# Optimization experiments

Hardware: AMD Instinct MI355X
Metric: run time of the kernel (lower is better)

The kernel has to match this reference:

```python
import jax, jax.numpy as jnp
import numpy as np

B, N, NPOINT, NSAMPLE = 8, 16384, 512, 64
RADIUS = 0.1
C_IN = 64
DIMS = [64, 64, 128]


def setup_inputs() -> dict:
    key = jax.random.key(0)
    ks = jax.random.split(key, 8)
    xyz = jax.random.uniform(ks[0], (B, N, 3), jnp.float32)          # points in unit cube
    features = jax.random.normal(ks[1], (B, C_IN, N), jnp.float32)   # (B, C, N) per GroupGatherByIndex
    dims = [3 + C_IN] + DIMS                                         # use_xyz_feature adds 3
    out = {"xyz": xyz, "features": features}
    for i in range(3):
        out[f"W{i+1}"] = jax.random.normal(ks[2 + i], (dims[i], dims[i + 1]), jnp.float32) / np.sqrt(dims[i])
        out[f"b{i+1}"] = jnp.zeros((dims[i + 1],), jnp.float32)
    return out


def furthest_point_sampling(xyz, npoint):
    # Iterative FPS starting at index 0 (matches CUDA kernel semantics).
    Bq, Nq, _ = xyz.shape
    barange = jnp.arange(Bq)

    def step(carry, _):
        dists, last = carry
        p = xyz[barange, last]                       # (B, 3)
        d = jnp.sum((xyz - p[:, None, :]) ** 2, -1)  # (B, N)
        dists = jnp.minimum(dists, d)
        nxt = jnp.argmax(dists, axis=1).astype(jnp.int32)
        return (dists, nxt), nxt

    init = (jnp.full((Bq, Nq), 1e10, xyz.dtype), jnp.zeros((Bq,), jnp.int32))
    _, idxs = jax.lax.scan(step, init, None, length=npoint - 1)
    return jnp.concatenate([jnp.zeros((Bq, 1), jnp.int32), idxs.T], axis=1)  # (B, npoint)


def ball_query(new_xyz, xyz, radius, nsample):
    # For each centroid, first nsample in-ball indices (ascending), padded with first hit.
    Nq = xyz.shape[1]
    d2 = jnp.sum((new_xyz[:, :, None, :] - xyz[:, None, :, :]) ** 2, -1)  # (B, npoint, N)
    cand = jnp.where(d2 < radius * radius, jnp.arange(Nq, dtype=jnp.int32), Nq)
    cand = jnp.sort(cand, axis=-1)[..., :nsample]                          # (B, npoint, nsample)
    first = jnp.where(cand[..., :1] == Nq, 0, cand[..., :1])
    return jnp.where(cand == Nq, first, cand)


def reference(xyz, features, W1, b1, W2, b2, W3, b3):
    fps_idx = furthest_point_sampling(xyz, NPOINT)                  # (B, npoint)
    new_xyz = jax.vmap(lambda p, i: p[i])(xyz, fps_idx)             # (B, npoint, 3)
    idx = ball_query(new_xyz, xyz, RADIUS, NSAMPLE)                 # (B, npoint, nsample)
    grouped_xyz = jax.vmap(lambda p, i: p[i])(xyz, idx)             # (B, npoint, nsample, 3)
    centered = grouped_xyz - new_xyz[:, :, None, :]                 # centroid subtract
    feats_n = jnp.transpose(features, (0, 2, 1))                    # (B, N, C)
    grouped_f = jax.vmap(lambda f, i: f[i])(feats_n, idx)           # (B, npoint, nsample, C)
    h = jnp.concatenate([centered, grouped_f], axis=-1)             # (B, npoint, nsample, 3+C)
    for W, b in ((W1, b1), (W2, b2), (W3, b3)):                     # pointwise 1x1-conv MLP + ReLU
        h = jax.nn.relu(h @ W + b)
    return jnp.max(h, axis=2)                                       # max-pool over nsample -> (B, npoint, C_out)
```

## Files before the change

kernel.cpp:

```cpp
#include <hip/hip_runtime.h>

#define NB 8
#define NPTS 16384
#define NPOINT 512
#define NSAMPLE 64
#define CIN 64

typedef float v2f __attribute__((ext_vector_type(2)));

template <int CTRL>
__device__ __forceinline__ float dpp_f(float x) {
    int xi = __builtin_bit_cast(int, x);
    int yi = __builtin_amdgcn_update_dpp(xi, xi, CTRL, 0xF, 0xF, false);
    return __builtin_bit_cast(float, yi);
}
template <int CTRL>
__device__ __forceinline__ int dpp_i(int x) {
    return __builtin_amdgcn_update_dpp(x, x, CTRL, 0xF, 0xF, false);
}

__device__ __forceinline__ float wave_max_f(float x) {
    x = fmaxf(x, dpp_f<0x111>(x));
    x = fmaxf(x, dpp_f<0x112>(x));
    x = fmaxf(x, dpp_f<0x114>(x));
    x = fmaxf(x, dpp_f<0x118>(x));
    x = fmaxf(x, dpp_f<0x142>(x));
    x = fmaxf(x, dpp_f<0x143>(x));
    return x;
}
__device__ __forceinline__ int wave_min_i(int x) {
    x = min(x, dpp_i<0x111>(x));
    x = min(x, dpp_i<0x112>(x));
    x = min(x, dpp_i<0x114>(x));
    x = min(x, dpp_i<0x118>(x));
    x = min(x, dpp_i<0x142>(x));
    x = min(x, dpp_i<0x143>(x));
    return x;
}

#define CMB(va, ia, vb, ib) { bool t_ = ((vb) > (va)) || (((vb) == (va)) && ((ib) < (ia))); \
                              if (t_) { (va) = (vb); (ia) = (ib); } }

__global__ __launch_bounds__(512) __attribute__((amdgpu_waves_per_eu(2, 2)))
void fps_transpose_kernel(
    const float* __restrict__ xyz, const float* __restrict__ feats,
    int* __restrict__ fps_idx, float* __restrict__ feats_t)
{
    __shared__ float t[64][65];
    __shared__ __align__(16) int s_pair[2][8][2];

    if (blockIdx.x >= NB) {
        int blk = blockIdx.x - NB;
        int b = blk & 7;
        int tile = blk >> 3;
        int n0 = tile * 64;
        int cc = threadIdx.x & 63, rr = threadIdx.x >> 6;
        const float* fb = feats + (size_t)b * CIN * NPTS;
        #pragma unroll
        for (int k = 0; k < 8; ++k) {
            int c = rr + k * 8;
            t[c][cc] = fb[(size_t)c * NPTS + n0 + cc];
        }
        __syncthreads();
        float* fo = feats_t + ((size_t)b * NPTS + n0) * CIN;
        #pragma unroll
        for (int k = 0; k < 8; ++k) {
            int n = rr + k * 8;
            fo[n * CIN + cc] = t[cc][n];
        }
        return;
    }

    const int b = blockIdx.x;
    const int tid = threadIdx.x;
    const int wv = tid >> 6, ln = tid & 63;
    const float* xb = xyz + (size_t)b * NPTS * 3;
    const int base = tid * 32;

    v2f px2[16], py2[16], pz2[16], dd2[16];
    {
        const float4* xb4 = (const float4*)(xb + (size_t)base * 3);
        #pragma unroll
        for (int q = 0; q < 8; ++q) {
            float4 f0 = xb4[3 * q + 0];
            float4 f1 = xb4[3 * q + 1];
            float4 f2 = xb4[3 * q + 2];
            px2[2 * q + 0] = (v2f){f0.x, f0.w};
            py2[2 * q + 0] = (v2f){f0.y, f1.x};
            pz2[2 * q + 0] = (v2f){f0.z, f1.y};
            px2[2 * q + 1] = (v2f){f1.z, f2.y};
            py2[2 * q + 1] = (v2f){f1.w, f2.z};
            pz2[2 * q + 1] = (v2f){f2.x, f2.w};
        }
        #pragma unroll
        for (int k = 0; k < 16; ++k) dd2[k] = (v2f){1e10f, 1e10f};
    }
    if (tid == 0) fps_idx[b * NPOINT] = 0;
    float cx = xb[0], cy = xb[1], cz = xb[2];
    __syncthreads();

    for (int j = 1; j < NPOINT; ++j) {
        #pragma clang fp contract(off)
        const int p = j & 1;
        v2f ncx = (v2f){-cx, -cx};
        v2f ncy = (v2f){-cy, -cy};
        v2f ncz = (v2f){-cz, -cz};
        float bm = -1.0f;
        #pragma unroll
        for (int k = 0; k < 16; ++k) {
            v2f dx = px2[k] + ncx;
            v2f dy = py2[k] + ncy;
            v2f dz = pz2[k] + ncz;
            v2f s1 = dx * dx + dy * dy;
            v2f d2 = s1 + dz * dz;
            v2f nd = __builtin_elementwise_min(dd2[k], d2);
            dd2[k] = nd;
            bm = fmaxf(bm, fmaxf(nd.x, nd.y));
        }
        float wm = wave_max_f(bm);
        float wmax = __builtin_bit_cast(float,
            __builtin_amdgcn_readlane(__builtin_bit_cast(int, wm), 63));
        int mk = 64;
        #pragma unroll
        for (int k = 15; k >= 0; --k) {
            mk = (dd2[k].y == wmax) ? (2 * k + 1) : mk;
            mk = (dd2[k].x == wmax) ? (2 * k)     : mk;
        }
        int mi = (mk == 64) ? 0x7fffffff : (base + mk);
        int rm = wave_min_i(mi);
        int wave_mi = __builtin_amdgcn_readlane(rm, 63);
        if (ln == 0) {
            s_pair[p][wv][0] = __builtin_bit_cast(int, wmax);
            s_pair[p][wv][1] = wave_mi;
        }
        __syncthreads();
        int4 q0 = *(const int4*)&s_pair[p][0][0];
        int4 q1 = *(const int4*)&s_pair[p][2][0];
        int4 q2 = *(const int4*)&s_pair[p][4][0];
        int4 q3 = *(const int4*)&s_pair[p][6][0];
        float v0 = __builtin_bit_cast(float, q0.x); int i0 = q0.y;
        float v1 = __builtin_bit_cast(float, q0.z); int i1 = q0.w;
        float v2 = __builtin_bit_cast(float, q1.x); int i2 = q1.y;
        float v3 = __builtin_bit_cast(float, q1.z); int i3 = q1.w;
        float v4 = __builtin_bit_cast(float, q2.x); int i4 = q2.y;
        float v5 = __builtin_bit_cast(float, q2.z); int i5 = q2.w;
        float v6 = __builtin_bit_cast(float, q3.x); int i6 = q3.y;
        float v7 = __builtin_bit_cast(float, q3.z); int i7 = q3.w;
        CMB(v0, i0, v1, i1); CMB(v2, i2, v3, i3);
        CMB(v4, i4, v5, i5); CMB(v6, i6, v7, i7);
        CMB(v0, i0, v2, i2); CMB(v4, i4, v6, i6);
        CMB(v0, i0, v4, i4);
        int ch = __builtin_amdgcn_readfirstlane(i0);
        const float* cp = xb + 3 * ch;
        cx = cp[0]; cy = cp[1]; cz = cp[2];
        if (tid == 0) fps_idx[b * NPOINT + j] = ch;
    }
}

__global__ __launch_bounds__(64) void ball_kernel(
    const float* __restrict__ xyz, const int* __restrict__ fps_idx, int* __restrict__ ball_idx)
{
    const float R2 = (float)(0.1 * 0.1);
    int blk = blockIdx.x;
    int b = blk & 7, j = blk >> 3;
    int lane = threadIdx.x;
    int cent = b * NPOINT + j;
    const float* xb = xyz + (size_t)b * NPTS * 3;
    int cidx = fps_idx[cent];
    float cx = xb[3 * cidx + 0];
    float cy = xb[3 * cidx + 1];
    float cz = xb[3 * cidx + 2];

    __shared__ int slots[64];
    int cnt = 0;
    for (int base = 0; base < NPTS; base += 64) {
        int i = base + lane;
        float dx = __fsub_rn(xb[3 * i + 0], cx);
        float dy = __fsub_rn(xb[3 * i + 1], cy);
        float dz = __fsub_rn(xb[3 * i + 2], cz);
        float d2 = __fadd_rn(__fadd_rn(__fmul_rn(dx, dx), __fmul_rn(dy, dy)), __fmul_rn(dz, dz));
        bool inb = d2 < R2;
        unsigned long long m = __ballot(inb);
        int pre = (int)__popcll(m & ((1ull << lane) - 1ull));
        int slot = cnt + pre;
        if (inb && slot < NSAMPLE) slots[slot] = i;
        cnt += (int)__popcll(m);
        if (cnt >= NSAMPLE) break;
    }
    __syncthreads();
    int first = (cnt > 0) ? slots[0] : 0;
    int v = (lane < cnt) ? slots[lane] : first;
    ball_idx[(size_t)cent * NSAMPLE + lane] = v;
}

__global__ __launch_bounds__(64) void mlp_kernel(
    const float* __restrict__ xyz, const float* __restrict__ feats_t,
    const int* __restrict__ fps_idx, const int* __restrict__ ball_idx,
    const float* __restrict__ W1, const float* __restrict__ b1,
    const float* __restrict__ W2, const float* __restrict__ b2,
    const float* __restrict__ W3, const float* __restrict__ b3,
    float* __restrict__ out)
{
    int blk = blockIdx.x;
    int b = blk & 7, j = blk >> 3;
    int s = threadIdx.x;
    int cent = b * NPOINT + j;

    __shared__ float X[67][64];

    int i = ball_idx[(size_t)cent * NSAMPLE + s];
    int cidx = fps_idx[cent];
    const float* cp = xyz + ((size_t)b * NPTS + cidx) * 3;
    float cx = cp[0], cy = cp[1], cz = cp[2];
    const float* pp = xyz + ((size_t)b * NPTS + i) * 3;
    X[64][s] = pp[0] - cx;
    X[65][s] = pp[1] - cy;
    X[66][s] = pp[2] - cz;
    const float4* fr = (const float4*)(feats_t + ((size_t)b * NPTS + i) * CIN);
    #pragma unroll
    for (int q = 0; q < 16; ++q) {
        float4 f = fr[q];
        X[q * 4 + 0][s] = f.x;
        X[q * 4 + 1][s] = f.y;
        X[q * 4 + 2][s] = f.z;
        X[q * 4 + 3][s] = f.w;
    }

    float acc[64];
    #pragma unroll
    for (int o = 0; o < 64; ++o) acc[o] = b1[o];
    for (int c = 0; c < 67; ++c) {
        float xc = X[c][s];
        const float* w = W1 + ((c < 64) ? (c + 3) : (c - 64)) * 64;
        #pragma unroll
        for (int o = 0; o < 64; ++o) acc[o] = fmaf(xc, w[o], acc[o]);
    }
    #pragma unroll
    for (int o = 0; o < 64; ++o) X[o][s] = fmaxf(acc[o], 0.0f);

    #pragma unroll
    for (int o = 0; o < 64; ++o) acc[o] = b2[o];
    for (int c = 0; c < 64; ++c) {
        float xc = X[c][s];
        const float* w = W2 + c * 64;
        #pragma unroll
        for (int o = 0; o < 64; ++o) acc[o] = fmaf(xc, w[o], acc[o]);
    }
    #pragma unroll
    for (int o = 0; o < 64; ++o) X[o][s] = fmaxf(acc[o], 0.0f);

    float h3[128];
    #pragma unroll
    for (int o = 0; o < 128; ++o) h3[o] = b3[o];
    for (int c = 0; c < 64; ++c) {
        float xc = X[c][s];
        const float* w = W3 + c * 128;
        #pragma unroll
        for (int o = 0; o < 128; ++o) h3[o] = fmaf(xc, w[o], h3[o]);
    }

    #pragma unroll
    for (int o = 0; o < 128; ++o) {
        float v = fmaxf(h3[o], 0.0f);
        #pragma unroll
        for (int off = 1; off < 64; off <<= 1) v = fmaxf(v, __shfl_xor(v, off));
        h3[o] = v;
    }
    if (s == 0) {
        float* op = out + (size_t)cent * 128;
        #pragma unroll
        for (int o = 0; o < 128; o += 4) {
            float4 v = make_float4(h3[o], h3[o + 1], h3[o + 2], h3[o + 3]);
            *(float4*)&op[o] = v;
        }
    }
}

extern "C" void kernel_launch(void* const* d_in, const int* in_sizes, int n_in,
                              void* d_out, int out_size, void* d_ws, size_t ws_size,
                              hipStream_t stream) {
    const float* xyz   = (const float*)d_in[0];
    const float* feats = (const float*)d_in[1];
    const float* W1 = (const float*)d_in[2];
    const float* b1 = (const float*)d_in[3];
    const float* W2 = (const float*)d_in[4];
    const float* b2 = (const float*)d_in[5];
    const float* W3 = (const float*)d_in[6];
    const float* b3 = (const float*)d_in[7];
    float* out = (float*)d_out;

    char* ws = (char*)d_ws;
    int*   fps_idx  = (int*)ws;
    int*   ball_idx = (int*)(ws + 16384);
    float* feats_t  = (float*)(ws + 16384 + 1048576);

    fps_transpose_kernel<<<NB + NB * (NPTS / 64), 512, 0, stream>>>(xyz, feats, fps_idx, feats_t);
    ball_kernel<<<NB * NPOINT, 64, 0, stream>>>(xyz, fps_idx, ball_idx);
    mlp_kernel<<<NB * NPOINT, 64, 0, stream>>>(xyz, feats_t, fps_idx, ball_idx,
                                               W1, b1, W2, b2, W3, b3, out);
}
```

Measured before the change: 1.190 ms.

## Spatially bucket points and prune FPS distance updates with per-thread bounding boxes

Adds a counting-sort kernel that buckets each batch's points into an 8x8x8 grid and writes them out as SoA coordinates plus original indices. FPS then loads spatially coherent points per thread, keeps a per-thread bounding box, and skips the distance update when the box cannot beat the thread's current max distance. The per-lane argmax scan is also skipped for lanes that do not hold the wave max. This targets the serial FPS loop's per-iteration arithmetic, at the cost of an extra launch and scattered global writes. Ties among equal distances may now resolve by sorted order rather than original index.

```diff
diff --git a/kernel.cpp b/kernel.cpp
--- a/kernel.cpp
+++ b/kernel.cpp
@@ -41,9 +41,53 @@
 #define CMB(va, ia, vb, ib) { bool t_ = ((vb) > (va)) || (((vb) == (va)) && ((ib) < (ia))); \
                               if (t_) { (va) = (vb); (ia) = (ib); } }
 
+__global__ __launch_bounds__(512) void sort_kernel(
+    const float* __restrict__ xyz,
+    float* __restrict__ xs, float* __restrict__ ys,
+    float* __restrict__ zs, int* __restrict__ sidx)
+{
+    const int b = blockIdx.x, tid = threadIdx.x;
+    const float* xb = xyz + (size_t)b * NPTS * 3;
+    __shared__ int hist[512];
+    __shared__ int cur[512];
+    hist[tid] = 0;
+    __syncthreads();
+    for (int k = 0; k < 32; ++k) {
+        int i = tid + k * 512;
+        float x = xb[3 * i], y = xb[3 * i + 1], z = xb[3 * i + 2];
+        int ix = min(7, (int)(x * 8.f)), iy = min(7, (int)(y * 8.f)), iz = min(7, (int)(z * 8.f));
+        atomicAdd(&hist[(ix << 6) | (iy << 3) | iz], 1);
+    }
+    __syncthreads();
+    cur[tid] = hist[tid];
+    __syncthreads();
+    for (int off = 1; off < 512; off <<= 1) {
+        int add = (tid >= off) ? hist[tid - off] : 0;
+        __syncthreads();
+        hist[tid] += add;
+        __syncthreads();
+    }
+    cur[tid] = hist[tid] - cur[tid];
+    __syncthreads();
+    float* xsb = xs + (size_t)b * NPTS;
+    float* ysb = ys + (size_t)b * NPTS;
+    float* zsb = zs + (size_t)b * NPTS;
+    int*   sib = sidx + (size_t)b * NPTS;
+    for (int k = 0; k < 32; ++k) {
+        int i = tid + k * 512;
+        float x = xb[3 * i], y = xb[3 * i + 1], z = xb[3 * i + 2];
+        int ix = min(7, (int)(x * 8.f)), iy = min(7, (int)(y * 8.f)), iz = min(7, (int)(z * 8.f));
+        int c = (ix << 6) | (iy << 3) | iz;
+        int pos = atomicAdd(&cur[c], 1);
+        xsb[pos] = x; ysb[pos] = y; zsb[pos] = z; sib[pos] = i;
+    }
+}
+
 __global__ __launch_bounds__(512) __attribute__((amdgpu_waves_per_eu(2, 2)))
 void fps_transpose_kernel(
     const float* __restrict__ xyz, const float* __restrict__ feats,
+    const float* __restrict__ xs, const float* __restrict__ ys,
+    const float* __restrict__ zs, const int* __restrict__ sidx,
     int* __restrict__ fps_idx, float* __restrict__ feats_t)
 {
     __shared__ float t[64][65];
@@ -74,27 +118,42 @@
     const int b = blockIdx.x;
     const int tid = threadIdx.x;
     const int wv = tid >> 6, ln = tid & 63;
-    const float* xb = xyz + (size_t)b * NPTS * 3;
+    const float* xb  = xyz + (size_t)b * NPTS * 3;
+    const float* xsb = xs + (size_t)b * NPTS;
+    const float* ysb = ys + (size_t)b * NPTS;
+    const float* zsb = zs + (size_t)b * NPTS;
+    const int*   sib = sidx + (size_t)b * NPTS;
     const int base = tid * 32;
 
     v2f px2[16], py2[16], pz2[16], dd2[16];
     {
-        const float4* xb4 = (const float4*)(xb + (size_t)base * 3);
+        const float4* X4 = (const float4*)(xsb + base);
+        const float4* Y4 = (const float4*)(ysb + base);
+        const float4* Z4 = (const float4*)(zsb + base);
         #pragma unroll
         for (int q = 0; q < 8; ++q) {
-            float4 f0 = xb4[3 * q + 0];
-            float4 f1 = xb4[3 * q + 1];
-            float4 f2 = xb4[3 * q + 2];
-            px2[2 * q + 0] = (v2f){f0.x, f0.w};
-            py2[2 * q + 0] = (v2f){f0.y, f1.x};
-            pz2[2 * q + 0] = (v2f){f0.z, f1.y};
-            px2[2 * q + 1] = (v2f){f1.z, f2.y};
-            py2[2 * q + 1] = (v2f){f1.w, f2.z};
-            pz2[2 * q + 1] = (v2f){f2.x, f2.w};
+            float4 fx = X4[q], fy = Y4[q], fz = Z4[q];
+            px2[2 * q + 0] = (v2f){fx.x, fx.y};  px2[2 * q + 1] = (v2f){fx.z, fx.w};
+            py2[2 * q + 0] = (v2f){fy.x, fy.y};  py2[2 * q + 1] = (v2f){fy.z, fy.w};
+            pz2[2 * q + 0] = (v2f){fz.x, fz.y};  pz2[2 * q + 1] = (v2f){fz.z, fz.w};
         }
         #pragma unroll
         for (int k = 0; k < 16; ++k) dd2[k] = (v2f){1e10f, 1e10f};
     }
+    float bxmin, bxmax, bymin, bymax, bzmin, bzmax;
+    {
+        v2f mnx = px2[0], mxx = px2[0], mny = py2[0], mxy = py2[0], mnz = pz2[0], mxz = pz2[0];
+        #pragma unroll
+        for (int k = 1; k < 16; ++k) {
+            mnx = __builtin_elementwise_min(mnx, px2[k]); mxx = __builtin_elementwise_max(mxx, px2[k]);
+            mny = __builtin_elementwise_min(mny, py2[k]); mxy = __builtin_elementwise_max(mxy, py2[k]);
+            mnz = __builtin_elementwise_min(mnz, pz2[k]); mxz = __builtin_elementwise_max(mxz, pz2[k]);
+        }
+        bxmin = fminf(mnx.x, mnx.y); bxmax = fmaxf(mxx.x, mxx.y);
+        bymin = fminf(mny.x, mny.y); bymax = fmaxf(mxy.x, mxy.y);
+        bzmin = fminf(mnz.x, mnz.y); bzmax = fmaxf(mxz.x, mxz.y);
+    }
+    float cm = 1e10f;
     if (tid == 0) fps_idx[b * NPOINT] = 0;
     float cx = xb[0], cy = xb[1], cz = xb[2];
     __syncthreads();
@@ -102,31 +161,42 @@
     for (int j = 1; j < NPOINT; ++j) {
         #pragma clang fp contract(off)
         const int p = j & 1;
-        v2f ncx = (v2f){-cx, -cx};
-        v2f ncy = (v2f){-cy, -cy};
-        v2f ncz = (v2f){-cz, -cz};
-        float bm = -1.0f;
-        #pragma unroll
-        for (int k = 0; k < 16; ++k) {
-            v2f dx = px2[k] + ncx;
-            v2f dy = py2[k] + ncy;
-            v2f dz = pz2[k] + ncz;
-            v2f s1 = dx * dx + dy * dy;
-            v2f d2 = s1 + dz * dz;
-            v2f nd = __builtin_elementwise_min(dd2[k], d2);
-            dd2[k] = nd;
-            bm = fmaxf(bm, fmaxf(nd.x, nd.y));
-        }
-        float wm = wave_max_f(bm);
+        float qx = cx - fminf(fmaxf(cx, bxmin), bxmax);
+        float qy = cy - fminf(fmaxf(cy, bymin), bymax);
+        float qz = cz - fminf(fmaxf(cz, bzmin), bzmax);
+        float bd2 = qx * qx + qy * qy + qz * qz;
+        bool upd = bd2 < cm * 1.0001f;
+        if (upd) {
+            v2f ncx = (v2f){-cx, -cx};
+            v2f ncy = (v2f){-cy, -cy};
+            v2f ncz = (v2f){-cz, -cz};
+            float bm = -1.0f;
+            #pragma unroll
+            for (int k = 0; k < 16; ++k) {
+                v2f dx = px2[k] + ncx;
+                v2f dy = py2[k] + ncy;
+                v2f dz = pz2[k] + ncz;
+                v2f s1 = dx * dx + dy * dy;
+                v2f d2 = s1 + dz * dz;
+                v2f nd = __builtin_elementwise_min(dd2[k], d2);
+                dd2[k] = nd;
+                bm = fmaxf(bm, fmaxf(nd.x, nd.y));
+            }
+            cm = bm;
+        }
+        float wm = wave_max_f(cm);
         float wmax = __builtin_bit_cast(float,
             __builtin_amdgcn_readlane(__builtin_bit_cast(int, wm), 63));
-        int mk = 64;
-        #pragma unroll
-        for (int k = 15; k >= 0; --k) {
-            mk = (dd2[k].y == wmax) ? (2 * k + 1) : mk;
-            mk = (dd2[k].x == wmax) ? (2 * k)     : mk;
-        }
-        int mi = (mk == 64) ? 0x7fffffff : (base + mk);
+        int mi = 0x7fffffff;
+        if (cm == wmax) {
+            int mk = 64;
+            #pragma unroll
+            for (int k = 15; k >= 0; --k) {
+                mk = (dd2[k].y == wmax) ? (2 * k + 1) : mk;
+                mk = (dd2[k].x == wmax) ? (2 * k)     : mk;
+            }
+            mi = base + mk;
+        }
         int rm = wave_min_i(mi);
         int wave_mi = __builtin_amdgcn_readlane(rm, 63);
         if (ln == 0) {
@@ -151,9 +221,8 @@
         CMB(v0, i0, v2, i2); CMB(v4, i4, v6, i6);
         CMB(v0, i0, v4, i4);
         int ch = __builtin_amdgcn_readfirstlane(i0);
-        const float* cp = xb + 3 * ch;
-        cx = cp[0]; cy = cp[1]; cz = cp[2];
-        if (tid == 0) fps_idx[b * NPOINT + j] = ch;
+        cx = xsb[ch]; cy = ysb[ch]; cz = zsb[ch];
+        if (tid == 0) fps_idx[b * NPOINT + j] = sib[ch];
     }
 }
 
@@ -291,10 +360,17 @@
 
     char* ws = (char*)d_ws;
     int*   fps_idx  = (int*)ws;
-    int*   ball_idx = (int*)(ws + 16384);
-    float* feats_t  = (float*)(ws + 16384 + 1048576);
-
-    fps_transpose_kernel<<<NB + NB * (NPTS / 64), 512, 0, stream>>>(xyz, feats, fps_idx, feats_t);
+    char*  shared_rgn = ws + 16384;
+    float* xs   = (float*)(shared_rgn);
+    float* ys   = (float*)(shared_rgn + 524288);
+    float* zs   = (float*)(shared_rgn + 2 * 524288);
+    int*   sidx = (int*)  (shared_rgn + 3 * 524288);
+    int*   ball_idx = (int*)shared_rgn;
+    float* feats_t  = (float*)(ws + 16384 + 4 * 524288);
+
+    sort_kernel<<<NB, 512, 0, stream>>>(xyz, xs, ys, zs, sidx);
+    fps_transpose_kernel<<<NB + NB * (NPTS / 64), 512, 0, stream>>>(
+        xyz, feats, xs, ys, zs, sidx, fps_idx, feats_t);
     ball_kernel<<<NB * NPOINT, 64, 0, stream>>>(xyz, fps_idx, ball_idx);
     mlp_kernel<<<NB * NPOINT, 64, 0, stream>>>(xyz, feats_t, fps_idx, ball_idx,
                                                W1, b1, W2, b2, W3, b3, out);
```

Result: slower. 1.282 ms (+7.8%).
